# Optimization experiments

Measured on AMD Instinct MI355X. Metric: run time of the kernel, lower is better.

Reference implementation:

```python
import jax, jax.numpy as jnp
import numpy as np

SQRT_2_OVER_PI = 0.7978845608028654

def gelu_new(x):
    # HF 'gelu_new': 0.5*x*(1+tanh(sqrt(2/pi)*(x+0.044715*x^3)))
    return 0.5 * x * (1.0 + jnp.tanh(SQRT_2_OVER_PI * (x + 0.044715 * x * x * x)))

def phm_linear(x, phm_rule, W_left, W_right, bias, n):
    # x: [..., n*p]; phm_rule: [n, n, n]; W_left: [n, p, r]; W_right: [n, r, q]
    # H = sum_i kron(phm_rule[i], W_i), W_i = W_left[i] @ W_right[i]; y = x @ H + b
    p = x.shape[-1] // n
    W = jnp.einsum('ipk,ikq->ipq', W_left, W_right)          # [n, p, q]
    xr = x.reshape(x.shape[:-1] + (n, p))                    # [..., n, p]
    # kron(A,B)[a*p+r, c*q+s] = A[a,c]*B[r,s]
    y = jnp.einsum('...ap,iac,ipq->...cq', xr, phm_rule, W)  # [..., n, q]
    y = y.reshape(x.shape[:-1] + (n * W.shape[-1],))
    return y + bias

def setup_inputs() -> dict:
    key = jax.random.key(0)
    ks = jax.random.split(key, 7)
    B, S, D, d, n = 8, 4096, 768, 192, 4
    x = jax.random.normal(ks[0], (B, S, D), dtype=jnp.float32)
    phm_rule_d = jax.random.normal(ks[1], (n, n, n), dtype=jnp.float32) * 0.01
    W_left_d = jax.random.normal(ks[2], (n, D // n, 1), dtype=jnp.float32) * 0.05
    W_right_d = jax.random.normal(ks[3], (n, 1, d // n), dtype=jnp.float32) * 0.05
    bias_d = jnp.zeros((d,), dtype=jnp.float32)
    phm_rule_u = jax.random.normal(ks[4], (n, n, n), dtype=jnp.float32) * 0.01
    W_left_u = jax.random.normal(ks[5], (n, d // n, 1), dtype=jnp.float32) * 0.05
    W_right_u = jax.random.normal(ks[6], (n, 1, D // n), dtype=jnp.float32) * 0.05
    bias_u = jnp.zeros((D,), dtype=jnp.float32)
    return {"x": x, "phm_rule_d": phm_rule_d, "W_left_d": W_left_d, "W_right_d": W_right_d,
            "bias_d": bias_d, "phm_rule_u": phm_rule_u, "W_left_u": W_left_u,
            "W_right_u": W_right_u, "bias_u": bias_u}

def reference(x, phm_rule_d, W_left_d, W_right_d, bias_d, phm_rule_u, W_left_u, W_right_u, bias_u):
    n = phm_rule_d.shape[0]
    z = phm_linear(x, phm_rule_d, W_left_d, W_right_d, bias_d, n)
    z = gelu_new(z)
    return phm_linear(z, phm_rule_u, W_left_u, W_right_u, bias_u, n)
```

## Files before the change

### kernel.cpp

```cpp
#include <hip/hip_runtime.h>
#include <math.h>


#define SQ2PI 0.79788456080286535588f

typedef float vfloat4 __attribute__((ext_vector_type(4)));
typedef unsigned int vuint2 __attribute__((ext_vector_type(2)));

template<int CTRL>
__device__ __forceinline__ float ror_add(float v) {
    int s = __builtin_amdgcn_update_dpp(0, __float_as_int(v), CTRL, 0xF, 0xF, true);
    return v + __int_as_float(s);
}
__device__ __forceinline__ float reduce16(float v) {
    v = ror_add<0x121>(v);
    v = ror_add<0x122>(v);
    v = ror_add<0x124>(v);
    v = ror_add<0x128>(v);
    return v;
}

__device__ __forceinline__ void swap16(float& d, float& s) {
    vuint2 t = __builtin_amdgcn_permlane16_swap(__float_as_uint(d), __float_as_uint(s), false, false);
    d = __uint_as_float(t.x);  s = __uint_as_float(t.y);
}
__device__ __forceinline__ void swap32(float& d, float& s) {
    vuint2 t = __builtin_amdgcn_permlane32_swap(__float_as_uint(d), __float_as_uint(s), false, false);
    d = __uint_as_float(t.x);  s = __uint_as_float(t.y);
}
__device__ __forceinline__ void bcast4(float h, float& b0, float& b1, float& b2, float& b3) {
    float y1 = h, y2 = h;
    swap16(y1, y2);
    b0 = y1; b2 = y1; swap32(b0, b2);
    b1 = y2; b3 = y2; swap32(b1, b3);
}

__device__ __forceinline__ void nt_store4(float* p, const float4& v) {
    vfloat4 nv;
    nv.x = v.x; nv.y = v.y; nv.z = v.z; nv.w = v.w;
    __builtin_nontemporal_store(nv, (vfloat4*)p);
}

__global__ __launch_bounds__(256)
void phm_fused(const float* __restrict__ x,
               const float* __restrict__ rule_d,
               const float* __restrict__ Wl_d,
               const float* __restrict__ Wr_d,
               const float* __restrict__ bias_d,
               const float* __restrict__ rule_u,
               const float* __restrict__ Wl_u,
               const float* __restrict__ Wr_u,
               const float* __restrict__ bias_u,
               float* __restrict__ out,
               int n_tokens)
{
    __shared__ __attribute__((aligned(16))) float sLd[768];
    __shared__ __attribute__((aligned(16))) float sRu[768];
    __shared__ __attribute__((aligned(16))) float sLu[192];
    __shared__ float sRuleD[64];
    __shared__ float sRuleU[64];

    const int tid = threadIdx.x;
    for (int i = tid; i < 768; i += 256) sLd[i] = Wl_d[i];
    for (int i = tid; i < 768; i += 256) sRu[i] = Wr_u[i];
    if (tid < 192)      sLu[tid]        = Wl_u[tid];
    if (tid < 64)       sRuleD[tid]     = rule_d[tid];
    else if (tid < 128) sRuleU[tid-64]  = rule_u[tid-64];

    const int lane = tid & 63;
    const int wave = tid >> 6;
    const int a    = lane >> 4;
    const int r    = lane & 15;
    const int off  = 192*a + 4*r;

    float bd[3];
    float rdw[4][3];
    float4 bu[3];
    #pragma unroll
    for (int w = 0; w < 3; ++w) bd[w] = bias_d[a*48 + 3*r + w];
    #pragma unroll
    for (int i = 0; i < 4; ++i)
        #pragma unroll
        for (int w = 0; w < 3; ++w) rdw[i][w] = Wr_d[i*48 + 3*r + w];
    #pragma unroll
    for (int u = 0; u < 3; ++u)
        bu[u] = *(const float4*)(bias_u + off + 64*u);

    __syncthreads();

    const int wid     = blockIdx.x * 4 + wave;
    const int n_waves = gridDim.x * 4;
    const int n_pairs = n_tokens >> 1;

    float4 A0[3], A1[3];
    {
        const int pr0 = (wid < n_pairs) ? wid : 0;
        const float* xp = x + (size_t)pr0 * 1536 + off;
        #pragma unroll
        for (int u = 0; u < 3; ++u) {
            A0[u] = *(const float4*)(xp + 64*u);
            A1[u] = *(const float4*)(xp + 768 + 64*u);
        }
    }

    for (int pr = wid; pr < n_pairs; pr += n_waves) {
        const int nx = pr + n_waves;
        const float* np = x + (size_t)(nx < n_pairs ? nx : pr) * 1536 + off;
        float4 B0[3], B1[3];
        #pragma unroll
        for (int u = 0; u < 3; ++u) {
            B0[u] = *(const float4*)(np + 64*u);
            B1[u] = *(const float4*)(np + 768 + 64*u);
        }

        float s0[4] = {0,0,0,0}, s1[4] = {0,0,0,0};
        #pragma unroll
        for (int u = 0; u < 3; ++u) {
            const float4 xa = A0[u];
            const float4 xb = A1[u];
            #pragma unroll
            for (int i = 0; i < 4; ++i) {
                const float4 lv = *(const float4*)&sLd[i*192 + 4*r + 64*u];
                s0[i] = fmaf(xa.x, lv.x, s0[i]);  s1[i] = fmaf(xb.x, lv.x, s1[i]);
                s0[i] = fmaf(xa.y, lv.y, s0[i]);  s1[i] = fmaf(xb.y, lv.y, s1[i]);
                s0[i] = fmaf(xa.z, lv.z, s0[i]);  s1[i] = fmaf(xb.z, lv.z, s1[i]);
                s0[i] = fmaf(xa.w, lv.w, s0[i]);  s1[i] = fmaf(xb.w, lv.w, s1[i]);
            }
        }

        float tD0[4], tD1[4];
        #pragma unroll
        for (int i = 0; i < 4; ++i) {
            const float rk0 = sRuleD[i*16 +  0 + a];
            const float rk1 = sRuleD[i*16 +  4 + a];
            const float rk2 = sRuleD[i*16 +  8 + a];
            const float rk3 = sRuleD[i*16 + 12 + a];
            float b0, b1, b2, b3;
            bcast4(reduce16(s0[i]), b0, b1, b2, b3);
            tD0[i] = fmaf(b0, rk0, fmaf(b1, rk1, fmaf(b2, rk2, b3 * rk3)));
            bcast4(reduce16(s1[i]), b0, b1, b2, b3);
            tD1[i] = fmaf(b0, rk0, fmaf(b1, rk1, fmaf(b2, rk2, b3 * rk3)));
        }

        float g0[3], g1[3];
        #pragma unroll
        for (int w = 0; w < 3; ++w) {
            float z0 = bd[w], z1 = bd[w];
            #pragma unroll
            for (int i = 0; i < 4; ++i) {
                z0 = fmaf(tD0[i], rdw[i][w], z0);
                z1 = fmaf(tD1[i], rdw[i][w], z1);
            }
            const float i0 = SQ2PI * fmaf(0.044715f*z0, z0*z0, z0);
            const float i1 = SQ2PI * fmaf(0.044715f*z1, z1*z1, z1);
            const float e0 = __expf(2.0f*i0);
            const float e1 = __expf(2.0f*i1);
            g0[w] = 0.5f*z0*(1.0f + (1.0f - 2.0f/(e0 + 1.0f)));
            g1[w] = 0.5f*z1*(1.0f + (1.0f - 2.0f/(e1 + 1.0f)));
        }

        float tU0[4], tU1[4];
        #pragma unroll
        for (int i = 0; i < 4; ++i) {
            const float l0 = sLu[i*48 + 3*r + 0];
            const float l1 = sLu[i*48 + 3*r + 1];
            const float l2 = sLu[i*48 + 3*r + 2];
            const float rk0 = sRuleU[i*16 +  0 + a];
            const float rk1 = sRuleU[i*16 +  4 + a];
            const float rk2 = sRuleU[i*16 +  8 + a];
            const float rk3 = sRuleU[i*16 + 12 + a];
            float a0 = g0[0]*l0 + g0[1]*l1 + g0[2]*l2;
            float a1 = g1[0]*l0 + g1[1]*l1 + g1[2]*l2;
            float b0, b1, b2, b3;
            bcast4(reduce16(a0), b0, b1, b2, b3);
            tU0[i] = fmaf(b0, rk0, fmaf(b1, rk1, fmaf(b2, rk2, b3 * rk3)));
            bcast4(reduce16(a1), b0, b1, b2, b3);
            tU1[i] = fmaf(b0, rk0, fmaf(b1, rk1, fmaf(b2, rk2, b3 * rk3)));
        }

        float* op = out + (size_t)pr * 1536 + off;
        #pragma unroll
        for (int u = 0; u < 3; ++u) {
            float4 ov0 = bu[u], ov1 = bu[u];
            #pragma unroll
            for (int i = 0; i < 4; ++i) {
                const float4 ru = *(const float4*)&sRu[i*192 + 4*r + 64*u];
                ov0.x = fmaf(tU0[i], ru.x, ov0.x);  ov1.x = fmaf(tU1[i], ru.x, ov1.x);
                ov0.y = fmaf(tU0[i], ru.y, ov0.y);  ov1.y = fmaf(tU1[i], ru.y, ov1.y);
                ov0.z = fmaf(tU0[i], ru.z, ov0.z);  ov1.z = fmaf(tU1[i], ru.z, ov1.z);
                ov0.w = fmaf(tU0[i], ru.w, ov0.w);  ov1.w = fmaf(tU1[i], ru.w, ov1.w);
            }
            nt_store4(op + 64*u,       ov0);
            nt_store4(op + 768 + 64*u, ov1);
        }

        #pragma unroll
        for (int u = 0; u < 3; ++u) { A0[u] = B0[u]; A1[u] = B1[u]; }
    }
}

extern "C" void kernel_launch(void* const* d_in, const int* in_sizes, int n_in,
                              void* d_out, int out_size, void* d_ws, size_t ws_size,
                              hipStream_t stream) {
    const float* x      = (const float*)d_in[0];
    const float* rule_d = (const float*)d_in[1];
    const float* Wl_d   = (const float*)d_in[2];
    const float* Wr_d   = (const float*)d_in[3];
    const float* bias_d = (const float*)d_in[4];
    const float* rule_u = (const float*)d_in[5];
    const float* Wl_u   = (const float*)d_in[6];
    const float* Wr_u   = (const float*)d_in[7];
    const float* bias_u = (const float*)d_in[8];
    float* out          = (float*)d_out;

    const int n_tokens = in_sizes[0] / 768;

    phm_fused<<<dim3(1024), dim3(256), 0, stream>>>(
        x, rule_d, Wl_d, Wr_d, bias_d, rule_u, Wl_u, Wr_u, bias_u, out, n_tokens);
}
```

Baseline: 194.7 us.

## Triple-buffer token-pair loads and move small weights from registers to LDS

Replaces the single-slot register prefetch with a three-slot rotating buffer, so up to three token-pair loads are in flight per wave while one pair is computed. To make room in registers, the down-projection bias, Wr_d and up-projection bias now live in LDS and are re-read on each iteration. This deepens memory-level parallelism on a bandwidth-bound kernel. The cost is extra LDS reads per pair and roughly 24 more live VGPRs for the extra slots, which may lower occupancy.

```diff
diff --git a/kernel.cpp b/kernel.cpp
--- a/kernel.cpp
+++ b/kernel.cpp
@@ -40,6 +40,8 @@
     nv.x = v.x; nv.y = v.y; nv.z = v.z; nv.w = v.w;
     __builtin_nontemporal_store(nv, (vfloat4*)p);
 }
+
+struct Slot { float4 a0[3]; float4 a1[3]; };
 
 __global__ __launch_bounds__(256)
 void phm_fused(const float* __restrict__ x,
@@ -56,14 +58,22 @@
 {
     __shared__ __attribute__((aligned(16))) float sLd[768];
     __shared__ __attribute__((aligned(16))) float sRu[768];
+    __shared__ __attribute__((aligned(16))) float sBu[768];
     __shared__ __attribute__((aligned(16))) float sLu[192];
+    __shared__ float sBd[192];
+    __shared__ float sRd[192];
     __shared__ float sRuleD[64];
     __shared__ float sRuleU[64];
 
     const int tid = threadIdx.x;
     for (int i = tid; i < 768; i += 256) sLd[i] = Wl_d[i];
     for (int i = tid; i < 768; i += 256) sRu[i] = Wr_u[i];
-    if (tid < 192)      sLu[tid]        = Wl_u[tid];
+    for (int i = tid; i < 768; i += 256) sBu[i] = bias_u[i];
+    if (tid < 192) {
+        sLu[tid] = Wl_u[tid];
+        sBd[tid] = bias_d[tid];
+        sRd[tid] = Wr_d[tid];
+    }
     if (tid < 64)       sRuleD[tid]     = rule_d[tid];
     else if (tid < 128) sRuleU[tid-64]  = rule_u[tid-64];
 
@@ -73,51 +83,27 @@
     const int r    = lane & 15;
     const int off  = 192*a + 4*r;
 
-    float bd[3];
-    float rdw[4][3];
-    float4 bu[3];
-    #pragma unroll
-    for (int w = 0; w < 3; ++w) bd[w] = bias_d[a*48 + 3*r + w];
-    #pragma unroll
-    for (int i = 0; i < 4; ++i)
-        #pragma unroll
-        for (int w = 0; w < 3; ++w) rdw[i][w] = Wr_d[i*48 + 3*r + w];
-    #pragma unroll
-    for (int u = 0; u < 3; ++u)
-        bu[u] = *(const float4*)(bias_u + off + 64*u);
-
     __syncthreads();
 
     const int wid     = blockIdx.x * 4 + wave;
     const int n_waves = gridDim.x * 4;
     const int n_pairs = n_tokens >> 1;
 
-    float4 A0[3], A1[3];
-    {
-        const int pr0 = (wid < n_pairs) ? wid : 0;
-        const float* xp = x + (size_t)pr0 * 1536 + off;
+    auto issue = [&](Slot& S, int p) {
+        const float* xp = x + (size_t)p * 1536 + off;
         #pragma unroll
         for (int u = 0; u < 3; ++u) {
-            A0[u] = *(const float4*)(xp + 64*u);
-            A1[u] = *(const float4*)(xp + 768 + 64*u);
-        }
-    }
-
-    for (int pr = wid; pr < n_pairs; pr += n_waves) {
-        const int nx = pr + n_waves;
-        const float* np = x + (size_t)(nx < n_pairs ? nx : pr) * 1536 + off;
-        float4 B0[3], B1[3];
+            S.a0[u] = *(const float4*)(xp + 64*u);
+            S.a1[u] = *(const float4*)(xp + 768 + 64*u);
+        }
+    };
+
+    auto compute_store = [&](Slot& S, int p) {
+        float s0[4] = {0,0,0,0}, s1[4] = {0,0,0,0};
         #pragma unroll
         for (int u = 0; u < 3; ++u) {
-            B0[u] = *(const float4*)(np + 64*u);
-            B1[u] = *(const float4*)(np + 768 + 64*u);
-        }
-
-        float s0[4] = {0,0,0,0}, s1[4] = {0,0,0,0};
-        #pragma unroll
-        for (int u = 0; u < 3; ++u) {
-            const float4 xa = A0[u];
-            const float4 xb = A1[u];
+            const float4 xa = S.a0[u];
+            const float4 xb = S.a1[u];
             #pragma unroll
             for (int i = 0; i < 4; ++i) {
                 const float4 lv = *(const float4*)&sLd[i*192 + 4*r + 64*u];
@@ -145,11 +131,12 @@
         float g0[3], g1[3];
         #pragma unroll
         for (int w = 0; w < 3; ++w) {
-            float z0 = bd[w], z1 = bd[w];
+            float z0 = sBd[a*48 + 3*r + w], z1 = z0;
             #pragma unroll
             for (int i = 0; i < 4; ++i) {
-                z0 = fmaf(tD0[i], rdw[i][w], z0);
-                z1 = fmaf(tD1[i], rdw[i][w], z1);
+                const float rd = sRd[i*48 + 3*r + w];
+                z0 = fmaf(tD0[i], rd, z0);
+                z1 = fmaf(tD1[i], rd, z1);
             }
             const float i0 = SQ2PI * fmaf(0.044715f*z0, z0*z0, z0);
             const float i1 = SQ2PI * fmaf(0.044715f*z1, z1*z1, z1);
@@ -178,10 +165,11 @@
             tU1[i] = fmaf(b0, rk0, fmaf(b1, rk1, fmaf(b2, rk2, b3 * rk3)));
         }
 
-        float* op = out + (size_t)pr * 1536 + off;
+        float* op = out + (size_t)p * 1536 + off;
         #pragma unroll
         for (int u = 0; u < 3; ++u) {
-            float4 ov0 = bu[u], ov1 = bu[u];
+            const float4 bv = *(const float4*)&sBu[off + 64*u];
+            float4 ov0 = bv, ov1 = bv;
             #pragma unroll
             for (int i = 0; i < 4; ++i) {
                 const float4 ru = *(const float4*)&sRu[i*192 + 4*r + 64*u];
@@ -193,10 +181,30 @@
             nt_store4(op + 64*u,       ov0);
             nt_store4(op + 768 + 64*u, ov1);
         }
-
-        #pragma unroll
-        for (int u = 0; u < 3; ++u) { A0[u] = B0[u]; A1[u] = B1[u]; }
+    };
+
+    int cnt = 0;
+    for (int p = wid; p < n_pairs; p += n_waves) ++cnt;
+
+    Slot S0, S1, S2;
+    if (cnt > 0)  issue(S0, wid);
+    if (cnt > 1)  issue(S1, wid + n_waves);
+    if (cnt > 2)  issue(S2, wid + 2*n_waves);
+
+    int pr = wid;
+    for (int k = 0; k + 2 < cnt; k += 3) {
+        compute_store(S0, pr);
+        if (k + 3 < cnt) issue(S0, pr + 3*n_waves);
+        compute_store(S1, pr + n_waves);
+        if (k + 4 < cnt) issue(S1, pr + 4*n_waves);
+        compute_store(S2, pr + 2*n_waves);
+        if (k + 5 < cnt) issue(S2, pr + 5*n_waves);
+        pr += 3*n_waves;
     }
+    const int rem = cnt % 3;
+    const int done = cnt - rem;
+    if (rem > 0) compute_store((done % 3 == 0) ? S0 : (done % 3 == 1) ? S1 : S2, pr);
+    if (rem > 1) compute_store((done % 3 == 0) ? S1 : (done % 3 == 1) ? S2 : S0, pr + n_waves);
 }
 
 extern "C" void kernel_launch(void* const* d_in, const int* in_sizes, int n_in,
```

Result: slower. 203.9 us (+4.7%).
